# Kernel tuning notes

Measured on AMD Instinct MI355X. Metric: run time of the kernel, lower is better.

Reference implementation:

```python
import jax, jax.numpy as jnp
import numpy as np

N = 8192          # number of nodes
F_IN = 256        # in_features
F_OUT = 128       # out_features


def setup_inputs() -> dict:
    key = jax.random.key(0)
    k1, k2, k3, k4 = jax.random.split(key, 4)
    input = jax.random.normal(k1, (N, F_IN), dtype=jnp.float32)
    adj = jax.random.uniform(k2, (N, N), dtype=jnp.float32)
    stdv = 1.0 / np.sqrt(F_OUT)
    weight = jax.random.uniform(k3, (F_IN, F_OUT), dtype=jnp.float32, minval=-stdv, maxval=stdv)
    bias = jax.random.uniform(k4, (F_OUT,), dtype=jnp.float32, minval=-stdv, maxval=stdv)
    return {"input": input, "adj": adj, "weight": weight, "bias": bias}


def reference(input, adj, weight, bias):
    # support = X @ W  [N, F_OUT]
    support = jnp.matmul(input, weight)
    # Subgraph block decomposition over a node partition is exactly A @ support:
    # block (k,i) computes adj[S_k][:, S_i] @ support[S_i] scatter-added into rows S_k.
    output = jnp.matmul(adj, support)  # [N, F_OUT]
    return output + bias
```

## Files before the change

kernel.cpp:

```cpp
#include <hip/hip_runtime.h>
#include <hip/hip_bf16.h>

#define N_NODES 8192
#define F_IN 256
#define F_OUT 128

#define SPLITK 4
#define KQ (N_NODES / SPLITK)
#define BK 64
#define NT (KQ / BK)
#define A_LDS 8192
#define B_LDS 16384
#define B_BASE (2 * A_LDS)
#define LDS_TOTAL (2 * A_LDS + 2 * B_LDS)

typedef __attribute__((ext_vector_type(4))) float f32x4;
typedef __attribute__((ext_vector_type(8))) short bf16x8;
typedef __attribute__((ext_vector_type(4))) unsigned int u32x4;

static __device__ __forceinline__ short bfr(float x) {
    __hip_bfloat16 h = __float2bfloat16(x);
    union { __hip_bfloat16 h; short s; } u; u.h = h;
    return u.s;
}

static __device__ __forceinline__ void gload16(const void* g, void* l) {
    __builtin_amdgcn_global_load_lds(
        (const __attribute__((address_space(1))) unsigned int*)g,
        (__attribute__((address_space(3))) unsigned int*)l, 16, 0, 0);
}

__global__ __launch_bounds__(256) void support_kernel(
        const float* __restrict__ X, const float* __restrict__ W,
        unsigned short* __restrict__ supT) {
    __shared__ float Xs[32][68];
    __shared__ float Ws[64][128];
    const int t = threadIdx.x;
    const int n0 = blockIdx.x * 32;
    const int tc = t & 31;
    const int tr = t >> 5;
    float acc[4][4];
    #pragma unroll
    for (int i = 0; i < 4; ++i)
        #pragma unroll
        for (int j = 0; j < 4; ++j) acc[i][j] = 0.f;

    for (int k0 = 0; k0 < F_IN; k0 += 64) {
        __syncthreads();
        {
            const int r = t >> 3, kc = (t & 7) * 8;
            const float* src = X + (size_t)(n0 + r) * F_IN + k0 + kc;
            f32x4 v0 = *(const f32x4*)src;
            f32x4 v1 = *(const f32x4*)(src + 4);
            *(f32x4*)&Xs[r][kc]     = v0;
            *(f32x4*)&Xs[r][kc + 4] = v1;
        }
        {
            const int col = t & 127, kb = t >> 7;
            #pragma unroll
            for (int i = 0; i < 32; ++i) {
                const int k = kb + i * 2;
                Ws[k][col] = W[(size_t)(k0 + k) * F_OUT + col];
            }
        }
        __syncthreads();
        #pragma unroll 8
        for (int k = 0; k < 64; ++k) {
            const f32x4 b = *(const f32x4*)&Ws[k][tc * 4];
            float a[4];
            #pragma unroll
            for (int i = 0; i < 4; ++i) a[i] = Xs[tr * 4 + i][k];
            #pragma unroll
            for (int i = 0; i < 4; ++i) {
                acc[i][0] += a[i] * b.x; acc[i][1] += a[i] * b.y;
                acc[i][2] += a[i] * b.z; acc[i][3] += a[i] * b.w;
            }
        }
    }
    #pragma unroll
    for (int j = 0; j < 4; ++j) {
        const int col = tc * 4 + j;
        #pragma unroll
        for (int i = 0; i < 4; ++i) {
            supT[(size_t)col * N_NODES + n0 + tr * 4 + i] =
                (unsigned short)bfr(acc[i][j]);
        }
    }
}

__global__ __launch_bounds__(512, 4) void gcn_kernel(
        const float* __restrict__ adj, const unsigned short* __restrict__ supT,
        const float* __restrict__ bias, float* __restrict__ out) {
    __shared__ char lds[LDS_TOTAL];
    const int t = threadIdx.x;
    const int l = t & 63;
    const int w = t >> 6;
    const int rb = blockIdx.x & 127;
    const int h = blockIdx.x >> 7;
    const int n0 = rb * 64;
    const int k0 = h * KQ;

    const int arow = 8 * w + (l >> 3);
    unsigned int aoffv = (unsigned)(((size_t)(n0 + arow) * N_NODES + k0
                                     + (l & 7) * 8) * 4);
    const int awoff = arow * 128 + (((l & 7) ^ ((l >> 3) & 7)) * 16);

    const char* gB0 = (const char*)supT
        + ((size_t)(16 * w + (l >> 3)) * N_NODES + k0) * 2 + (((l & 7) ^ (l >> 3)) * 16);
    const char* gB1 = gB0 + (size_t)8 * N_NODES * 2;
    const int b_d0 = w * 2048;
    const int b_d1 = b_d0 + 1024;

    const int wm = w >> 2, wn = w & 3;
    const int aoff0 = (wm * 32 + (l & 15)) * 128;
    const int aoff1 = aoff0 + 16 * 128;
    const int akey = l & 7;
    const int boff0 = (wn * 32 + (l & 15)) * 128;
    const int boff1 = boff0 + 16 * 128;
    const int bkey = l & 7;
    const int cg = l >> 4;

    f32x4 acc00 = {0.f,0.f,0.f,0.f}, acc01 = {0.f,0.f,0.f,0.f};
    f32x4 acc10 = {0.f,0.f,0.f,0.f}, acc11 = {0.f,0.f,0.f,0.f};

    f32x4 aE0, aE1, aO0, aO1;

#define PK(dst, a, b) \
    asm("v_cvt_pk_bf16_f32 %0, %1, %2" : "=v"(dst) : "v"(a), "v"(b))

#define BLDA(dst, imm) \
    asm volatile("global_load_dwordx4 %0, %1, %2 offset:" imm \
                 : "=v"(dst) : "v"(aoffv), "s"(adj) : "memory")

#define STAGE_AREG(r0, r1) { \
    BLDA(r0, "0"); \
    BLDA(r1, "16"); \
    aoffv += 256; }

#define STAGE_B(P) { \
    char* bb = &lds[B_BASE + (P) * B_LDS]; \
    gload16(gB0, bb + b_d0); \
    gload16(gB1, bb + b_d1); \
    gB0 += 128; gB1 += 128; }

#define CVT_WRITE(WP, r0, r1) { \
    u32x4 q; \
    PK(q.x, r0.x, r0.y); PK(q.y, r0.z, r0.w); \
    PK(q.z, r1.x, r1.y); PK(q.w, r1.z, r1.w); \
    *(u32x4*)(&lds[(WP) * A_LDS] + awoff) = q; }

#define COMPUTE(P) { \
    const char* ab = &lds[(P) * A_LDS]; \
    const char* bb = &lds[B_BASE + (P) * B_LDS]; \
    _Pragma("unroll") \
    for (int ks = 0; ks < 2; ++ks) { \
        const int c = ks * 4 + cg; \
        bf16x8 a0 = *(const bf16x8*)(ab + aoff0 + ((c ^ akey) * 16)); \
        bf16x8 a1 = *(const bf16x8*)(ab + aoff1 + ((c ^ akey) * 16)); \
        bf16x8 b0 = *(const bf16x8*)(bb + boff0 + ((c ^ bkey) * 16)); \
        bf16x8 b1 = *(const bf16x8*)(bb + boff1 + ((c ^ bkey) * 16)); \
        acc00 = __builtin_amdgcn_mfma_f32_16x16x32_bf16(a0, b0, acc00, 0, 0, 0); \
        acc01 = __builtin_amdgcn_mfma_f32_16x16x32_bf16(a0, b1, acc01, 0, 0, 0); \
        acc10 = __builtin_amdgcn_mfma_f32_16x16x32_bf16(a1, b0, acc10, 0, 0, 0); \
        acc11 = __builtin_amdgcn_mfma_f32_16x16x32_bf16(a1, b1, acc11, 0, 0, 0); \
    } }

#define WAIT(IMM) { \
    asm volatile("s_waitcnt vmcnt(" IMM ")" ::: "memory"); \
    __builtin_amdgcn_sched_barrier(0); }

#define WAITL(IMM) { \
    asm volatile("s_waitcnt vmcnt(" IMM ") lgkmcnt(0)" ::: "memory"); \
    __builtin_amdgcn_sched_barrier(0); }

#define BAR() { \
    __builtin_amdgcn_s_barrier(); \
    __builtin_amdgcn_sched_barrier(0); }

    STAGE_AREG(aE0, aE1);
    STAGE_B(0);
    STAGE_AREG(aO0, aO1);
    WAIT("4");
    CVT_WRITE(0, aE0, aE1);
    WAITL("2");
    BAR();

    for (int t2 = 0; t2 + 3 < NT; t2 += 2) {
        STAGE_B(1);
        STAGE_AREG(aE0, aE1);
        COMPUTE(0);
        WAIT("4");
        CVT_WRITE(1, aO0, aO1);
        WAITL("2");
        BAR();
        STAGE_B(0);
        STAGE_AREG(aO0, aO1);
        COMPUTE(1);
        WAIT("4");
        CVT_WRITE(0, aE0, aE1);
        WAITL("2");
        BAR();
    }
    STAGE_B(1);
    COMPUTE(0);
    WAIT("2");
    CVT_WRITE(1, aO0, aO1);
    WAITL("0");
    BAR();
    COMPUTE(1);

#undef PK
#undef BLDA
#undef STAGE_AREG
#undef STAGE_B
#undef CVT_WRITE
#undef COMPUTE
#undef WAIT
#undef WAITL
#undef BAR

    const int col = wn * 32 + (l & 15);
    const int row0 = n0 + wm * 32 + (l >> 4) * 4;
    const float bv0 = (h == 0) ? bias[col]      : 0.0f;
    const float bv1 = (h == 0) ? bias[col + 16] : 0.0f;
    #pragma unroll
    for (int i = 0; i < 4; ++i) {
        float* o0 = out + (size_t)(row0 + i) * F_OUT + col;
        float* o1 = out + (size_t)(row0 + i + 16) * F_OUT + col;
        unsafeAtomicAdd(&o0[0],  acc00[i] + bv0);
        unsafeAtomicAdd(&o0[16], acc01[i] + bv1);
        unsafeAtomicAdd(&o1[0],  acc10[i] + bv0);
        unsafeAtomicAdd(&o1[16], acc11[i] + bv1);
    }
}

extern "C" void kernel_launch(void* const* d_in, const int* in_sizes, int n_in,
                              void* d_out, int out_size, void* d_ws, size_t ws_size,
                              hipStream_t stream) {
    const float* input  = (const float*)d_in[0];
    const float* adj    = (const float*)d_in[1];
    const float* weight = (const float*)d_in[2];
    const float* bias   = (const float*)d_in[3];
    float* out = (float*)d_out;
    unsigned short* supT = (unsigned short*)d_ws;

    hipMemsetAsync(d_out, 0, (size_t)out_size * sizeof(float), stream);
    support_kernel<<<N_NODES / 32, 256, 0, stream>>>(input, weight, supT);
    gcn_kernel<<<128 * SPLITK, 512, 0, stream>>>(adj, supT, bias, out);
}
```

Baseline: 79.87 us.

## Double row tile to 128 and raise split-K to 8 in GCN aggregation

Doubles the row tile of the adj@support kernel so each wave computes a 64x32 output slab, halving how often each support tile is re-read. Split-K is raised from 4 to 8 to keep the grid size constant. The A prefetch pipeline becomes single-stage with wider per-thread loads. The trade-offs are more atomic output traffic, larger LDS per block that reduces occupancy, and shallower load prefetching.

```diff
diff --git a/kernel.cpp b/kernel.cpp
--- a/kernel.cpp
+++ b/kernel.cpp
@@ -5,14 +5,14 @@
 #define F_IN 256
 #define F_OUT 128
 
-#define SPLITK 4
+#define SPLITK 8
 #define KQ (N_NODES / SPLITK)
 #define BK 64
 #define NT (KQ / BK)
-#define A_LDS 8192
+#define BM 128
+#define A_LDS 16384
 #define B_LDS 16384
-#define B_BASE (2 * A_LDS)
-#define LDS_TOTAL (2 * A_LDS + 2 * B_LDS)
+#define BUFB (A_LDS + B_LDS)
 
 typedef __attribute__((ext_vector_type(4))) float f32x4;
 typedef __attribute__((ext_vector_type(8))) short bf16x8;
@@ -91,19 +91,22 @@
 __global__ __launch_bounds__(512, 4) void gcn_kernel(
         const float* __restrict__ adj, const unsigned short* __restrict__ supT,
         const float* __restrict__ bias, float* __restrict__ out) {
-    __shared__ char lds[LDS_TOTAL];
+    __shared__ char lds[2 * BUFB];
     const int t = threadIdx.x;
     const int l = t & 63;
     const int w = t >> 6;
-    const int rb = blockIdx.x & 127;
-    const int h = blockIdx.x >> 7;
-    const int n0 = rb * 64;
+    const int rb = blockIdx.x & 63;
+    const int h = blockIdx.x >> 6;
+    const int n0 = rb * BM;
     const int k0 = h * KQ;
 
-    const int arow = 8 * w + (l >> 3);
-    unsigned int aoffv = (unsigned)(((size_t)(n0 + arow) * N_NODES + k0
-                                     + (l & 7) * 8) * 4);
-    const int awoff = arow * 128 + (((l & 7) ^ ((l >> 3) & 7)) * 16);
+    const int arow = t >> 2;
+    const int atq = t & 3;
+    unsigned int aoffv = (unsigned)((size_t)(n0 + arow) * N_NODES + k0) * 4
+                       + (unsigned)(atq * 64);
+    const int akw = arow & 7;
+    const int awoff0 = arow * 128 + (((atq * 2)     ^ akw) * 16);
+    const int awoff1 = arow * 128 + (((atq * 2 + 1) ^ akw) * 16);
 
     const char* gB0 = (const char*)supT
         + ((size_t)(16 * w + (l >> 3)) * N_NODES + k0) * 2 + (((l & 7) ^ (l >> 3)) * 16);
@@ -112,125 +115,128 @@
     const int b_d1 = b_d0 + 1024;
 
     const int wm = w >> 2, wn = w & 3;
-    const int aoff0 = (wm * 32 + (l & 15)) * 128;
-    const int aoff1 = aoff0 + 16 * 128;
     const int akey = l & 7;
+    int aoffm[4];
+    #pragma unroll
+    for (int m = 0; m < 4; ++m)
+        aoffm[m] = (wm * 64 + 16 * m + (l & 15)) * 128;
     const int boff0 = (wn * 32 + (l & 15)) * 128;
     const int boff1 = boff0 + 16 * 128;
     const int bkey = l & 7;
     const int cg = l >> 4;
 
-    f32x4 acc00 = {0.f,0.f,0.f,0.f}, acc01 = {0.f,0.f,0.f,0.f};
-    f32x4 acc10 = {0.f,0.f,0.f,0.f}, acc11 = {0.f,0.f,0.f,0.f};
-
-    f32x4 aE0, aE1, aO0, aO1;
+    f32x4 acc[4][2];
+    #pragma unroll
+    for (int m = 0; m < 4; ++m)
+        #pragma unroll
+        for (int n = 0; n < 2; ++n) acc[m][n] = {0.f, 0.f, 0.f, 0.f};
+
+    f32x4 aR0, aR1, aR2, aR3;
 
 #define PK(dst, a, b) \
     asm("v_cvt_pk_bf16_f32 %0, %1, %2" : "=v"(dst) : "v"(a), "v"(b))
 
-#define BLDA(dst, imm) \
+#define LDA(dst, imm) \
     asm volatile("global_load_dwordx4 %0, %1, %2 offset:" imm \
                  : "=v"(dst) : "v"(aoffv), "s"(adj) : "memory")
 
-#define STAGE_AREG(r0, r1) { \
-    BLDA(r0, "0"); \
-    BLDA(r1, "16"); \
+#define STAGE_A() { \
+    LDA(aR0, "0"); LDA(aR1, "16"); LDA(aR2, "32"); LDA(aR3, "48"); \
     aoffv += 256; }
 
 #define STAGE_B(P) { \
-    char* bb = &lds[B_BASE + (P) * B_LDS]; \
+    char* bb = &lds[(P) * BUFB + A_LDS]; \
     gload16(gB0, bb + b_d0); \
     gload16(gB1, bb + b_d1); \
     gB0 += 128; gB1 += 128; }
 
-#define CVT_WRITE(WP, r0, r1) { \
-    u32x4 q; \
-    PK(q.x, r0.x, r0.y); PK(q.y, r0.z, r0.w); \
-    PK(q.z, r1.x, r1.y); PK(q.w, r1.z, r1.w); \
-    *(u32x4*)(&lds[(WP) * A_LDS] + awoff) = q; }
+#define CVT_WRITE(P) { \
+    u32x4 q0, q1; \
+    PK(q0.x, aR0.x, aR0.y); PK(q0.y, aR0.z, aR0.w); \
+    PK(q0.z, aR1.x, aR1.y); PK(q0.w, aR1.z, aR1.w); \
+    PK(q1.x, aR2.x, aR2.y); PK(q1.y, aR2.z, aR2.w); \
+    PK(q1.z, aR3.x, aR3.y); PK(q1.w, aR3.z, aR3.w); \
+    char* ab = &lds[(P) * BUFB]; \
+    *(u32x4*)(ab + awoff0) = q0; \
+    *(u32x4*)(ab + awoff1) = q1; }
 
 #define COMPUTE(P) { \
-    const char* ab = &lds[(P) * A_LDS]; \
-    const char* bb = &lds[B_BASE + (P) * B_LDS]; \
+    const char* ab = &lds[(P) * BUFB]; \
+    const char* bb = ab + A_LDS; \
     _Pragma("unroll") \
     for (int ks = 0; ks < 2; ++ks) { \
         const int c = ks * 4 + cg; \
-        bf16x8 a0 = *(const bf16x8*)(ab + aoff0 + ((c ^ akey) * 16)); \
-        bf16x8 a1 = *(const bf16x8*)(ab + aoff1 + ((c ^ akey) * 16)); \
-        bf16x8 b0 = *(const bf16x8*)(bb + boff0 + ((c ^ bkey) * 16)); \
-        bf16x8 b1 = *(const bf16x8*)(bb + boff1 + ((c ^ bkey) * 16)); \
-        acc00 = __builtin_amdgcn_mfma_f32_16x16x32_bf16(a0, b0, acc00, 0, 0, 0); \
-        acc01 = __builtin_amdgcn_mfma_f32_16x16x32_bf16(a0, b1, acc01, 0, 0, 0); \
-        acc10 = __builtin_amdgcn_mfma_f32_16x16x32_bf16(a1, b0, acc10, 0, 0, 0); \
-        acc11 = __builtin_amdgcn_mfma_f32_16x16x32_bf16(a1, b1, acc11, 0, 0, 0); \
+        bf16x8 bf0 = *(const bf16x8*)(bb + boff0 + ((c ^ bkey) * 16)); \
+        bf16x8 bf1 = *(const bf16x8*)(bb + boff1 + ((c ^ bkey) * 16)); \
+        _Pragma("unroll") \
+        for (int m = 0; m < 4; ++m) { \
+            bf16x8 af = *(const bf16x8*)(ab + aoffm[m] + ((c ^ akey) * 16)); \
+            acc[m][0] = __builtin_amdgcn_mfma_f32_16x16x32_bf16(af, bf0, acc[m][0], 0, 0, 0); \
+            acc[m][1] = __builtin_amdgcn_mfma_f32_16x16x32_bf16(af, bf1, acc[m][1], 0, 0, 0); \
+        } \
     } }
 
 #define WAIT(IMM) { \
     asm volatile("s_waitcnt vmcnt(" IMM ")" ::: "memory"); \
     __builtin_amdgcn_sched_barrier(0); }
 
-#define WAITL(IMM) { \
-    asm volatile("s_waitcnt vmcnt(" IMM ") lgkmcnt(0)" ::: "memory"); \
+#define WAITL0() { \
+    asm volatile("s_waitcnt vmcnt(0) lgkmcnt(0)" ::: "memory"); \
     __builtin_amdgcn_sched_barrier(0); }
 
 #define BAR() { \
     __builtin_amdgcn_s_barrier(); \
     __builtin_amdgcn_sched_barrier(0); }
 
-    STAGE_AREG(aE0, aE1);
+    STAGE_A();
     STAGE_B(0);
-    STAGE_AREG(aO0, aO1);
-    WAIT("4");
-    CVT_WRITE(0, aE0, aE1);
-    WAITL("2");
+    WAIT("2");
+    CVT_WRITE(0);
+    WAITL0();
     BAR();
 
-    for (int t2 = 0; t2 + 3 < NT; t2 += 2) {
+    for (int t2 = 0; t2 < NT; t2 += 2) {
+        STAGE_A();
         STAGE_B(1);
-        STAGE_AREG(aE0, aE1);
         COMPUTE(0);
-        WAIT("4");
-        CVT_WRITE(1, aO0, aO1);
-        WAITL("2");
+        WAIT("2");
+        CVT_WRITE(1);
+        WAITL0();
         BAR();
-        STAGE_B(0);
-        STAGE_AREG(aO0, aO1);
-        COMPUTE(1);
-        WAIT("4");
-        CVT_WRITE(0, aE0, aE1);
-        WAITL("2");
-        BAR();
-    }
-    STAGE_B(1);
-    COMPUTE(0);
-    WAIT("2");
-    CVT_WRITE(1, aO0, aO1);
-    WAITL("0");
-    BAR();
+        if (t2 + 2 < NT) {
+            STAGE_A();
+            STAGE_B(0);
+            COMPUTE(1);
+            WAIT("2");
+            CVT_WRITE(0);
+            WAITL0();
+            BAR();
+        }
+    }
     COMPUTE(1);
 
 #undef PK
-#undef BLDA
-#undef STAGE_AREG
+#undef LDA
+#undef STAGE_A
 #undef STAGE_B
 #undef CVT_WRITE
 #undef COMPUTE
 #undef WAIT
-#undef WAITL
+#undef WAITL0
 #undef BAR
 
     const int col = wn * 32 + (l & 15);
-    const int row0 = n0 + wm * 32 + (l >> 4) * 4;
     const float bv0 = (h == 0) ? bias[col]      : 0.0f;
     const float bv1 = (h == 0) ? bias[col + 16] : 0.0f;
-    #pragma unroll
-    for (int i = 0; i < 4; ++i) {
-        float* o0 = out + (size_t)(row0 + i) * F_OUT + col;
-        float* o1 = out + (size_t)(row0 + i + 16) * F_OUT + col;
-        unsafeAtomicAdd(&o0[0],  acc00[i] + bv0);
-        unsafeAtomicAdd(&o0[16], acc01[i] + bv1);
-        unsafeAtomicAdd(&o1[0],  acc10[i] + bv0);
-        unsafeAtomicAdd(&o1[16], acc11[i] + bv1);
+    const int rbase = n0 + wm * 64 + (l >> 4) * 4;
+    #pragma unroll
+    for (int m = 0; m < 4; ++m) {
+        #pragma unroll
+        for (int i = 0; i < 4; ++i) {
+            float* o = out + (size_t)(rbase + 16 * m + i) * F_OUT + col;
+            unsafeAtomicAdd(&o[0],  acc[m][0][i] + bv0);
+            unsafeAtomicAdd(&o[16], acc[m][1][i] + bv1);
+        }
     }
 }
 
@@ -246,5 +252,5 @@
 
     hipMemsetAsync(d_out, 0, (size_t)out_size * sizeof(float), stream);
     support_kernel<<<N_NODES / 32, 256, 0, stream>>>(input, weight, supT);
-    gcn_kernel<<<128 * SPLITK, 512, 0, stream>>>(adj, supT, bias, out);
-}
+    gcn_kernel<<<64 * SPLITK, 512, 0, stream>>>(adj, supT, bias, out);
+}
```

Measured after the change: 88.01 us. 10.2% more time.
